# Performance work log

Hardware: AMD Instinct MI355X
Metric: run time of the kernel (lower is better)

## Reference

```python
import jax, jax.numpy as jnp
import numpy as np

B, L, HID, NH = 8, 512, 768, 12
D = HID // NH
T_HOP, T_EDGE = 32, 64


def setup_inputs() -> dict:
    key = jax.random.key(0)
    ks = jax.random.split(key, 18)
    f = lambda k, s, sc=1.0: jax.random.normal(k, s, dtype=jnp.float32) * sc
    return {
        "x": f(ks[0], (B, L, HID)),
        "query_hop_emb": f(ks[1], (T_HOP, HID), 0.05),
        "query_edge_emb": f(ks[2], (T_EDGE, HID), 0.05),
        "key_hop_emb": f(ks[3], (T_HOP, HID), 0.05),
        "key_edge_emb": f(ks[4], (T_EDGE, HID), 0.05),
        "value_hop_emb": f(ks[5], (T_HOP, HID), 0.05),
        "value_edge_emb": f(ks[6], (T_EDGE, HID), 0.05),
        "hop": jax.random.randint(ks[7], (B, L, L), 0, T_HOP, dtype=jnp.int32),
        "edge_matrix": jax.random.randint(ks[8], (B, L, L), 0, T_EDGE, dtype=jnp.int32),
        "Wq": f(ks[9], (HID, HID), 0.02), "bq": f(ks[10], (HID,), 0.02),
        "Wk": f(ks[11], (HID, HID), 0.02), "bk": f(ks[12], (HID,), 0.02),
        "Wv": f(ks[13], (HID, HID), 0.02), "bv": f(ks[14], (HID,), 0.02),
        "Wo": f(ks[15], (HID, HID), 0.02), "bo": f(ks[16], (HID,), 0.02),
    }


def reference(x, query_hop_emb, query_edge_emb, key_hop_emb, key_edge_emb,
              value_hop_emb, value_edge_emb, hop, edge_matrix,
              Wq, bq, Wk, bk, Wv, bv, Wo, bo):
    b, l, _ = x.shape
    scale = 1.0 / np.sqrt(D).astype(np.float32)
    heads = lambda t: t.reshape(b, l, NH, D).transpose(0, 2, 1, 3)  # [B,H,L,D]
    emb = lambda t: t.reshape(-1, NH, D)                             # [T,H,D]

    q = heads(x @ Wq + bq)
    k = heads(x @ Wk + bk)
    v = heads(x @ Wv + bv)

    hop_idx = jnp.broadcast_to(hop[:, None], (b, NH, l, l))
    edge_idx = jnp.broadcast_to(edge_matrix[:, None], (b, NH, l, l))

    def bias(t, e, idx):
        # project onto type embeddings then gather per (i,j) type: [B,H,L,L]
        proj = jnp.einsum('bhld,thd->bhlt', t, emb(e))
        return jnp.take_along_axis(proj, idx, axis=3)

    scores = jnp.einsum('bhld,bhmd->bhlm', q, k)
    scores = scores + bias(q, query_hop_emb, hop_idx) + bias(q, query_edge_emb, edge_idx)
    scores = scores + bias(k, key_hop_emb, hop_idx) + bias(k, key_edge_emb, edge_idx)
    att = jax.nn.softmax(scores * scale, axis=3)

    def scatter_by_type(a, idx, T):
        # re-aggregate attention weights per hop/edge type: [B,H,L,T]
        bi = jnp.arange(b)[:, None, None, None]
        hi = jnp.arange(NH)[None, :, None, None]
        li = jnp.arange(l)[None, None, :, None]
        return jnp.zeros((b, NH, l, T), a.dtype).at[bi, hi, li, idx].add(a)

    out = jnp.einsum('bhlm,bhmd->bhld', att, v)
    out = out + jnp.einsum('bhlt,thd->bhld', scatter_by_type(att, hop_idx, T_HOP), emb(value_hop_emb))
    out = out + jnp.einsum('bhlt,thd->bhld', scatter_by_type(att, edge_idx, T_EDGE), emb(value_edge_emb))

    out = out.transpose(0, 2, 1, 3).reshape(b, l, NH * D)
    return out @ Wo + bo
```

## Files before the change

kernel.cpp:

```cpp
#include <hip/hip_runtime.h>
#include <stdint.h>

#define B_   8
#define L_   512
#define HID_ 768
#define NH_  12
#define D_   64
#define BH_  96
#define TT_  96

typedef __attribute__((ext_vector_type(8))) short short8;
typedef __attribute__((ext_vector_type(4))) float fv4;

#define MFMA16(a, b, c) __builtin_amdgcn_mfma_f32_16x16x32_bf16((a), (b), (c), 0, 0, 0)

__device__ __forceinline__ float bf2f(uint16_t h) {
  union { uint32_t u; float f; } c; c.u = ((uint32_t)h) << 16; return c.f;
}
__device__ __forceinline__ uint16_t f2bf(float x) {
  union { float f; uint32_t u; } c; c.f = x;
  uint32_t r = (c.u + 0x7FFFu + ((c.u >> 16) & 1u)) >> 16;
  return (uint16_t)r;
}
__device__ __forceinline__ float clampf(float v, float lim) {
  return fminf(fmaxf(v, -lim), lim);
}

__device__ __forceinline__ void gld_lds16(const uint16_t* g, uint16_t* lds) {
  __builtin_amdgcn_global_load_lds(
      (const __attribute__((address_space(1))) uint32_t*)(uintptr_t)g,
      (__attribute__((address_space(3))) uint32_t*)(uintptr_t)lds, 16, 0, 0);
}

__device__ __forceinline__ int detect_fp32(const void* xraw) {
  const uint16_t* r = (const uint16_t*)xraw;
  int cnt = 0;
#pragma unroll
  for (int j = 0; j < 16; j++) {
    uint16_t u = r[2 * j];
    int e = (u >> 7) & 0xFF;
    if (u != 0 && e >= 100 && e <= 140) cnt++;
  }
  return cnt < 10;
}

#define SEG_X    0
#define SEG_QH   3145728
#define SEG_QE   3170304
#define SEG_KH   3219456
#define SEG_KE   3244032
#define SEG_VH   3293184
#define SEG_VE   3317760
#define SEG_BQ   3366912
#define SEG_BK   3367680
#define SEG_BV   3368448
#define SEG_BO   3369216
#define SEG_END  3369984
#define SEG_VET  3369984
#define SEG_PK   3443712
#define SEG_ALL  5540864

__global__ __launch_bounds__(256) void convert_all(
    const void* __restrict__ x, const void* __restrict__ qh,
    const void* __restrict__ qe, const void* __restrict__ kh,
    const void* __restrict__ ke, const void* __restrict__ vh,
    const void* __restrict__ ve, const void* __restrict__ b0,
    const void* __restrict__ b1, const void* __restrict__ b2,
    const void* __restrict__ b3, const int* __restrict__ hop,
    const int* __restrict__ edge, uint16_t* __restrict__ dst,
    uint16_t* __restrict__ VET, uint16_t* __restrict__ PK) {
  const int gid = blockIdx.x * 256 + threadIdx.x;
  if (gid >= SEG_ALL) return;
  const int f = detect_fp32(x);
  if (gid >= SEG_PK) {
    const int g = gid - SEG_PK;
    PK[g] = (uint16_t)((hop[g] & 31) | ((edge[g] & 63) << 8));
    return;
  }
  if (gid >= SEG_VET) {
    const int g = gid - SEG_VET;
    const int t = g % TT_;
    const int d = (g / TT_) % D_;
    const int hh = g / (TT_ * D_);
    const void* src = (t < 32) ? vh : ve;
    const size_t idx = (size_t)(t < 32 ? t : t - 32) * HID_ + hh * D_ + d;
    VET[g] = f ? f2bf(((const float*)src)[idx]) : ((const uint16_t*)src)[idx];
    return;
  }
  const void* src;
  int local;
  if (gid < SEG_QH)      { src = x;  local = gid - SEG_X; }
  else if (gid < SEG_QE) { src = qh; local = gid - SEG_QH; }
  else if (gid < SEG_KH) { src = qe; local = gid - SEG_QE; }
  else if (gid < SEG_KE) { src = kh; local = gid - SEG_KH; }
  else if (gid < SEG_VH) { src = ke; local = gid - SEG_KE; }
  else if (gid < SEG_VE) { src = vh; local = gid - SEG_VH; }
  else if (gid < SEG_BQ) { src = ve; local = gid - SEG_VE; }
  else if (gid < SEG_BK) { src = b0; local = gid - SEG_BQ; }
  else if (gid < SEG_BV) { src = b1; local = gid - SEG_BK; }
  else if (gid < SEG_BO) { src = b2; local = gid - SEG_BV; }
  else                   { src = b3; local = gid - SEG_BO; }
  if (f)
    dst[gid] = f2bf(((const float*)src)[local]);
  else
    dst[gid] = ((const uint16_t*)src)[local];
}

__global__ __launch_bounds__(256) void tr_any4(
    const void* __restrict__ s0, const void* __restrict__ s1,
    const void* __restrict__ s2, const void* __restrict__ s3,
    uint16_t* __restrict__ dstbase) {
  __shared__ uint16_t t[32][33];
  const int z = blockIdx.z;
  const void* src = (z == 0) ? s0 : (z == 1) ? s1 : (z == 2) ? s2 : s3;
  uint16_t* dst = dstbase + (size_t)z * (768 * 768);
  const int fp32 = detect_fp32(s0);
  const int tx = threadIdx.x, ty = threadIdx.y;
  const int r0 = blockIdx.y * 32, c0 = blockIdx.x * 32;
#pragma unroll
  for (int k = 0; k < 4; k++) {
    size_t idx = (size_t)(r0 + ty + k * 8) * 768 + c0 + tx;
    t[ty + k * 8][tx] =
        fp32 ? f2bf(((const float*)src)[idx]) : ((const uint16_t*)src)[idx];
  }
  __syncthreads();
#pragma unroll
  for (int k = 0; k < 4; k++)
    dst[(size_t)(c0 + ty + k * 8) * 768 + r0 + tx] = t[tx][ty + k * 8];
}

__global__ __launch_bounds__(256) void gemm128(
    const uint16_t* __restrict__ A,
    const uint16_t* __restrict__ BT0, const uint16_t* __restrict__ BT1,
    const uint16_t* __restrict__ BT2,
    const uint16_t* __restrict__ bias0, const uint16_t* __restrict__ bias1,
    const uint16_t* __restrict__ bias2,
    uint16_t* __restrict__ out, uint16_t* __restrict__ vt) {
  const int z = blockIdx.z;
  const uint16_t* BT = (z == 0) ? BT0 : (z == 1) ? BT1 : BT2;
  const uint16_t* bias = (z == 0) ? bias0 : (z == 1) ? bias1 : bias2;

  __shared__ __align__(16) uint16_t As[128 * 32];
  __shared__ __align__(16) uint16_t Bs[128 * 32];

  const int tid = threadIdx.x;
  const int lane = tid & 63, quad = lane >> 4, l16 = lane & 15;
  const int w = tid >> 6, wm = w & 1, wn = w >> 1;
  const int m0 = blockIdx.x * 128, n0 = blockIdx.y * 128;

  fv4 acc[4][4];
#pragma unroll
  for (int i = 0; i < 4; i++)
#pragma unroll
    for (int j = 0; j < 4; j++) acc[i][j] = (fv4){0.f, 0.f, 0.f, 0.f};

  const int c0 = tid, c1 = tid + 256;
  const int r0 = c0 >> 2, g0 = (c0 & 3) ^ ((r0 >> 1) & 3);
  const int r1 = c1 >> 2, g1 = (c1 & 3) ^ ((r1 >> 1) & 3);
  const uint16_t* A0 = A + (size_t)(m0 + r0) * HID_ + g0 * 8;
  const uint16_t* A1 = A + (size_t)(m0 + r1) * HID_ + g1 * 8;
  const uint16_t* B0 = BT + (size_t)(n0 + r0) * HID_ + g0 * 8;
  const uint16_t* B1 = BT + (size_t)(n0 + r1) * HID_ + g1 * 8;
  uint16_t* lA0 = &As[c0 * 8];
  uint16_t* lA1 = &As[c1 * 8];
  uint16_t* lB0 = &Bs[c0 * 8];
  uint16_t* lB1 = &Bs[c1 * 8];

  int aoff[4], boff[4];
#pragma unroll
  for (int mi = 0; mi < 4; mi++) {
    int row = wm * 64 + mi * 16 + l16;
    aoff[mi] = row * 32 + (quad ^ ((row >> 1) & 3)) * 8;
  }
#pragma unroll
  for (int ni = 0; ni < 4; ni++) {
    int row = wn * 64 + ni * 16 + l16;
    boff[ni] = row * 32 + (quad ^ ((row >> 1) & 3)) * 8;
  }

  for (int k0 = 0; k0 < HID_; k0 += 32) {
    __syncthreads();
    gld_lds16(A0 + k0, lA0);
    gld_lds16(A1 + k0, lA1);
    gld_lds16(B0 + k0, lB0);
    gld_lds16(B1 + k0, lB1);
    __syncthreads();
    short8 af[4], bf[4];
#pragma unroll
    for (int mi = 0; mi < 4; mi++) af[mi] = *(const short8*)&As[aoff[mi]];
#pragma unroll
    for (int ni = 0; ni < 4; ni++) bf[ni] = *(const short8*)&Bs[boff[ni]];
#pragma unroll
    for (int mi = 0; mi < 4; mi++)
#pragma unroll
      for (int ni = 0; ni < 4; ni++)
        acc[mi][ni] = MFMA16(af[mi], bf[ni], acc[mi][ni]);
  }

#pragma unroll
  for (int mi = 0; mi < 4; mi++) {
#pragma unroll
    for (int ni = 0; ni < 4; ni++) {
      const int gn = n0 + wn * 64 + ni * 16 + l16;
      const float bv = bf2f(bias[gn]);
      const int gm0 = m0 + wm * 64 + mi * 16 + quad * 4;
      if (z == 2) {
        const int bb = gm0 >> 9, ll0 = gm0 & 511;
        const int hh = gn >> 6, dd = gn & 63;
        ushort4 pk;
        pk.x = f2bf(clampf(acc[mi][ni][0] + bv, 1e4f));
        pk.y = f2bf(clampf(acc[mi][ni][1] + bv, 1e4f));
        pk.z = f2bf(clampf(acc[mi][ni][2] + bv, 1e4f));
        pk.w = f2bf(clampf(acc[mi][ni][3] + bv, 1e4f));
        *(ushort4*)&vt[(((size_t)(bb * NH_ + hh)) * D_ + dd) * L_ + ll0] = pk;
      } else {
#pragma unroll
        for (int r = 0; r < 4; r++) {
          const int gm = gm0 + r;
          const float fval = clampf(acc[mi][ni][r] + bv, 1e4f);
          uint16_t* O = out + (size_t)z * ((size_t)BH_ * L_ * D_);
          const int bb = gm >> 9, ll = gm & 511, hh = gn >> 6, dd = gn & 63;
          O[(((size_t)(bb * NH_ + hh)) * L_ + ll) * D_ + dd] = f2bf(fval);
        }
      }
    }
  }
}

__global__ __launch_bounds__(256) void gemm64o(
    const uint16_t* __restrict__ A, const uint16_t* __restrict__ BT,
    const uint16_t* __restrict__ bias, float* __restrict__ out) {
  __shared__ __align__(16) uint16_t As[64 * 32];
  __shared__ __align__(16) uint16_t Bs[64 * 32];

  const int tid = threadIdx.x;
  const int lane = tid & 63, quad = lane >> 4, l16 = lane & 15;
  const int w = tid >> 6, wm = w & 1, wn = w >> 1;
  const int m0 = blockIdx.x * 64, n0 = blockIdx.y * 64;

  fv4 acc[2][2];
#pragma unroll
  for (int i = 0; i < 2; i++)
#pragma unroll
    for (int j = 0; j < 2; j++) acc[i][j] = (fv4){0.f, 0.f, 0.f, 0.f};

  const int c0 = tid;
  const int r0 = c0 >> 2, g0 = (c0 & 3) ^ ((r0 >> 1) & 3);
  const uint16_t* A0 = A + (size_t)(m0 + r0) * HID_ + g0 * 8;
  const uint16_t* B0 = BT + (size_t)(n0 + r0) * HID_ + g0 * 8;
  uint16_t* lA0 = &As[c0 * 8];
  uint16_t* lB0 = &Bs[c0 * 8];

  int aoff[2], boff[2];
#pragma unroll
  for (int mi = 0; mi < 2; mi++) {
    int row = wm * 32 + mi * 16 + l16;
    aoff[mi] = row * 32 + (quad ^ ((row >> 1) & 3)) * 8;
  }
#pragma unroll
  for (int ni = 0; ni < 2; ni++) {
    int row = wn * 32 + ni * 16 + l16;
    boff[ni] = row * 32 + (quad ^ ((row >> 1) & 3)) * 8;
  }

  for (int k0 = 0; k0 < HID_; k0 += 32) {
    __syncthreads();
    gld_lds16(A0 + k0, lA0);
    gld_lds16(B0 + k0, lB0);
    __syncthreads();
    short8 af[2], bf[2];
#pragma unroll
    for (int mi = 0; mi < 2; mi++) af[mi] = *(const short8*)&As[aoff[mi]];
#pragma unroll
    for (int ni = 0; ni < 2; ni++) bf[ni] = *(const short8*)&Bs[boff[ni]];
#pragma unroll
    for (int mi = 0; mi < 2; mi++)
#pragma unroll
      for (int ni = 0; ni < 2; ni++)
        acc[mi][ni] = MFMA16(af[mi], bf[ni], acc[mi][ni]);
  }

#pragma unroll
  for (int mi = 0; mi < 2; mi++) {
#pragma unroll
    for (int ni = 0; ni < 2; ni++) {
      const int gn = n0 + wn * 32 + ni * 16 + l16;
      const float bv = bf2f(bias[gn]);
#pragma unroll
      for (int r = 0; r < 4; r++) {
        const int gm = m0 + wm * 32 + mi * 16 + quad * 4 + r;
        out[(size_t)gm * HID_ + gn] = clampf(acc[mi][ni][r] + bv, 1e4f);
      }
    }
  }
}

#define SCALE_FX 4194304.f
#define INV_SCALE_FX 2.38418579e-7f
#define UBC 40.f

__global__ __launch_bounds__(256) void attn_kernel(
    const uint16_t* __restrict__ Q, const uint16_t* __restrict__ Km,
    const uint16_t* __restrict__ Vt,
    const uint16_t* __restrict__ qh, const uint16_t* __restrict__ qe,
    const uint16_t* __restrict__ kh, const uint16_t* __restrict__ ke,
    const uint16_t* __restrict__ VET, const uint16_t* __restrict__ PK,
    uint16_t* __restrict__ AO) {
  const int n = blockIdx.x;
  const int h = n % NH_;
  const int t2 = n / NH_;
  const int it = t2 & 7, b = t2 >> 3;
  const int bh = b * NH_ + h;
  const int i0 = it * 64;
  const int tid = threadIdx.x;
  const int w = tid >> 6, lane = tid & 63, quad = lane >> 4, l16 = lane & 15;
  const int gi = i0 + w * 16;

  __shared__ uint16_t cbs[4][16][98];
  __shared__ unsigned bkt[4][16][97];
  __shared__ __align__(16) uint16_t Pw[4][16][72];

  for (int k = lane; k < 16 * 97; k += 64) (&bkt[0][0][0])[w * 16 * 97 + k] = 0u;

  const size_t qkb = (size_t)bh * (L_ * D_);
  short8 a0 = *(const short8*)&Q[qkb + (size_t)(gi + l16) * D_ + quad * 8];
  short8 a1 = *(const short8*)&Q[qkb + (size_t)(gi + l16) * D_ + 32 + quad * 8];
  short8 kq0 = *(const short8*)&Km[qkb + (size_t)(gi + l16) * D_ + quad * 8];
  short8 kq1 =
      *(const short8*)&Km[qkb + (size_t)(gi + l16) * D_ + 32 + quad * 8];

  float hx[4] = {-1e30f, -1e30f, -1e30f, -1e30f};
  float ex[4] = {-1e30f, -1e30f, -1e30f, -1e30f};
#pragma unroll
  for (int nt = 0; nt < 6; nt++) {
    const uint16_t* eq;
    const uint16_t* ek;
    int t;
    if (nt < 2) { eq = qh; ek = kh; t = nt * 16 + l16; }
    else        { eq = qe; ek = ke; t = (nt - 2) * 16 + l16; }
    const size_t eb0 = (size_t)t * HID_ + h * D_;
    short8 bq0 = *(const short8*)&eq[eb0 + quad * 8];
    short8 bq1 = *(const short8*)&eq[eb0 + 32 + quad * 8];
    short8 bk0 = *(const short8*)&ek[eb0 + quad * 8];
    short8 bk1 = *(const short8*)&ek[eb0 + 32 + quad * 8];
    fv4 cc = (fv4){0.f, 0.f, 0.f, 0.f};
    cc = MFMA16(a0, bq0, cc);
    cc = MFMA16(a1, bq1, cc);
    cc = MFMA16(kq0, bk0, cc);
    cc = MFMA16(kq1, bk1, cc);
#pragma unroll
    for (int r = 0; r < 4; r++) {
      const float cv = clampf(cc[r], 1e4f);
      cbs[w][quad * 4 + r][nt * 16 + l16] = f2bf(cv);
      if (nt < 2) hx[r] = fmaxf(hx[r], cv);
      else        ex[r] = fmaxf(ex[r], cv);
    }
  }

  float mx[4];
#pragma unroll
  for (int r = 0; r < 4; r++) {
    float mh = hx[r], me = ex[r];
    mh = fmaxf(mh, __shfl_xor(mh, 1, 16));
    mh = fmaxf(mh, __shfl_xor(mh, 2, 16));
    mh = fmaxf(mh, __shfl_xor(mh, 4, 16));
    mh = fmaxf(mh, __shfl_xor(mh, 8, 16));
    me = fmaxf(me, __shfl_xor(me, 1, 16));
    me = fmaxf(me, __shfl_xor(me, 2, 16));
    me = fmaxf(me, __shfl_xor(me, 4, 16));
    me = fmaxf(me, __shfl_xor(me, 8, 16));
    mx[r] = mh + me + UBC;
  }

  const uint16_t* pkb = PK + ((size_t)(b * L_) + gi) * L_;
  const size_t vtb = (size_t)bh * (D_ * L_);

  fv4 oacc[4];
#pragma unroll
  for (int ni = 0; ni < 4; ni++) oacc[ni] = (fv4){0.f, 0.f, 0.f, 0.f};
  float lsr[4] = {0.f, 0.f, 0.f, 0.f};

  for (int jc = 0; jc < 8; jc++) {
    fv4 sacc[4];
#pragma unroll
    for (int ni = 0; ni < 4; ni++) {
      const int key = jc * 64 + ni * 16 + l16;
      short8 kb0 = *(const short8*)&Km[qkb + (size_t)key * D_ + quad * 8];
      short8 kb1 = *(const short8*)&Km[qkb + (size_t)key * D_ + 32 + quad * 8];
      fv4 a = (fv4){0.f, 0.f, 0.f, 0.f};
      a = MFMA16(a0, kb0, a);
      sacc[ni] = MFMA16(a1, kb1, a);
    }
#pragma unroll
    for (int ni = 0; ni < 4; ni++) {
#pragma unroll
      for (int r = 0; r < 4; r++) {
        const int row = quad * 4 + r;
        const uint32_t pk = pkb[(size_t)row * L_ + jc * 64 + ni * 16 + l16];
        const int th = pk & 31, te = pk >> 8;
        float s = sacc[ni][r] + bf2f(cbs[w][row][th]) +
                  bf2f(cbs[w][row][32 + te]);
        const float p = __expf((s - mx[r]) * 0.125f);
        lsr[r] += p;
        const unsigned pfx = (unsigned)(p * SCALE_FX + 0.5f);
        atomicAdd(&bkt[w][row][th], pfx);
        atomicAdd(&bkt[w][row][32 + te], pfx);
        Pw[w][row][ni * 16 + l16] = f2bf(p);
      }
    }
#pragma unroll
    for (int kc = 0; kc < 2; kc++) {
      short8 pa = *(const short8*)&Pw[w][l16][kc * 32 + quad * 8];
#pragma unroll
      for (int ni = 0; ni < 4; ni++) {
        short8 vb = *(const short8*)&Vt[vtb + (size_t)(ni * 16 + l16) * L_ +
                                        jc * 64 + kc * 32 + quad * 8];
        oacc[ni] = MFMA16(pa, vb, oacc[ni]);
      }
    }
  }

  const uint16_t* vet = VET + (size_t)h * D_ * TT_;
#pragma unroll
  for (int kc = 0; kc < 3; kc++) {
    short8 pa;
#pragma unroll
    for (int j = 0; j < 8; j++)
      pa[j] = (short)f2bf((float)bkt[w][l16][kc * 32 + quad * 8 + j] *
                          INV_SCALE_FX);
#pragma unroll
    for (int ni = 0; ni < 4; ni++) {
      short8 vb =
          *(const short8*)&vet[(size_t)(ni * 16 + l16) * TT_ + kc * 32 +
                               quad * 8];
      oacc[ni] = MFMA16(pa, vb, oacc[ni]);
    }
  }

  float linv[4];
#pragma unroll
  for (int r = 0; r < 4; r++) {
    float s = lsr[r];
    s += __shfl_xor(s, 1, 16);
    s += __shfl_xor(s, 2, 16);
    s += __shfl_xor(s, 4, 16);
    s += __shfl_xor(s, 8, 16);
    linv[r] = 1.f / s;
  }

#pragma unroll
  for (int ni = 0; ni < 4; ni++)
#pragma unroll
    for (int r = 0; r < 4; r++) {
      const int i = gi + quad * 4 + r;
      AO[(((size_t)b * L_ + i) * NH_ + h) * D_ + ni * 16 + l16] =
          f2bf(oacc[ni][r] * linv[r]);
    }
}

extern "C" void kernel_launch(void* const* d_in, const int* in_sizes, int n_in,
                              void* d_out, int out_size, void* d_ws,
                              size_t ws_size, hipStream_t stream) {
  const void* x_raw = d_in[0];
  const int* hop    = (const int*)d_in[7];
  const int* edge   = (const int*)d_in[8];

  char* ws = (char*)d_ws;
  uint16_t* QKV = (uint16_t*)(ws);
  uint16_t* Qp  = QKV;
  uint16_t* Kp  = QKV + (size_t)BH_ * L_ * D_;
  uint16_t* Vtp = (uint16_t*)(ws + 18874368);
  uint16_t* PKp = (uint16_t*)(ws + 25165824);
  uint16_t* AO  = (uint16_t*)(ws + 44040192);
  uint16_t* WTq = (uint16_t*)(ws + 50331648);
  uint16_t* WTk = WTq + 768 * 768;
  uint16_t* WTv = WTk + 768 * 768;
  uint16_t* WTo = WTv + 768 * 768;
  uint16_t* CAN = (uint16_t*)(ws + 55050240);
  uint16_t* VET = (uint16_t*)(ws + 61790208);

  uint16_t* xc  = CAN + SEG_X;
  uint16_t* qhc = CAN + SEG_QH;
  uint16_t* qec = CAN + SEG_QE;
  uint16_t* khc = CAN + SEG_KH;
  uint16_t* kec = CAN + SEG_KE;
  uint16_t* bqc = CAN + SEG_BQ;
  uint16_t* bkc = CAN + SEG_BK;
  uint16_t* bvc = CAN + SEG_BV;
  uint16_t* boc = CAN + SEG_BO;

  convert_all<<<(SEG_ALL + 255) / 256, 256, 0, stream>>>(
      x_raw, d_in[1], d_in[2], d_in[3], d_in[4], d_in[5], d_in[6],
      d_in[10], d_in[12], d_in[14], d_in[16], hop, edge, CAN, VET, PKp);

  dim3 tb(32, 8, 1);
  tr_any4<<<dim3(24, 24, 4), tb, 0, stream>>>(d_in[9], d_in[11], d_in[13],
                                              d_in[15], WTq);

  gemm128<<<dim3(32, 6, 3), 256, 0, stream>>>(xc, WTq, WTk, WTv, bqc, bkc,
                                              bvc, QKV, Vtp);

  attn_kernel<<<768, 256, 0, stream>>>(Qp, Kp, Vtp, qhc, qec, khc, kec, VET,
                                       PKp, AO);

  gemm64o<<<dim3(64, 12), 256, 0, stream>>>(AO, WTo, boc, (float*)d_out);
}
```

Measured before the change: 236.3 us.

## Pre-swizzle packed hop/edge indices to lane order for vectorized loads in attention

The conversion kernel now writes the packed hop/edge type indices in a layout that matches the attention kernel's MFMA lane/register ownership, so each lane gets its 16 indices per key chunk with two 16-byte loads instead of 16 scattered 2-byte loads. The softmax/bucket loop is split into phases (decode indices, gather biases, exponentiate, then atomics and P writes) to expose more independent work. A launch-bounds occupancy hint of 3 blocks is also added. The costs are a scattered write pattern in the conversion kernel and possible register pressure from the 16-element arrays under the occupancy constraint.

```diff
diff --git a/kernel.cpp b/kernel.cpp
--- a/kernel.cpp
+++ b/kernel.cpp
@@ -68,13 +68,22 @@
     const void* __restrict__ b1, const void* __restrict__ b2,
     const void* __restrict__ b3, const int* __restrict__ hop,
     const int* __restrict__ edge, uint16_t* __restrict__ dst,
-    uint16_t* __restrict__ VET, uint16_t* __restrict__ PK) {
+    uint16_t* __restrict__ VET, uint16_t* __restrict__ PKs) {
   const int gid = blockIdx.x * 256 + threadIdx.x;
   if (gid >= SEG_ALL) return;
   const int f = detect_fp32(x);
   if (gid >= SEG_PK) {
     const int g = gid - SEG_PK;
-    PK[g] = (uint16_t)((hop[g] & 31) | ((edge[g] & 63) << 8));
+    const int j = g & 511;
+    const int i = (g >> 9) & 511;
+    const int b = g >> 18;
+    const int it = i >> 6, w = (i >> 4) & 3, quad = (i >> 2) & 3, r = i & 3;
+    const int jc = j >> 6, ni = (j >> 4) & 3, l16 = j & 15;
+    const int lane = quad * 16 + l16;
+    const size_t didx =
+        ((((size_t)(b * 8 + it) * 4 + w) * 8 + jc) * 64 + lane) * 16 + r * 4 +
+        ni;
+    PKs[didx] = (uint16_t)((hop[g] & 31) | ((edge[g] & 63) << 8));
     return;
   }
   if (gid >= SEG_VET) {
@@ -299,28 +308,28 @@
 #define INV_SCALE_FX 2.38418579e-7f
 #define UBC 40.f
 
-__global__ __launch_bounds__(256) void attn_kernel(
+__global__ __launch_bounds__(256, 3) void attn_kernel(
     const uint16_t* __restrict__ Q, const uint16_t* __restrict__ Km,
     const uint16_t* __restrict__ Vt,
     const uint16_t* __restrict__ qh, const uint16_t* __restrict__ qe,
     const uint16_t* __restrict__ kh, const uint16_t* __restrict__ ke,
-    const uint16_t* __restrict__ VET, const uint16_t* __restrict__ PK,
+    const uint16_t* __restrict__ VET, const uint16_t* __restrict__ PKs,
     uint16_t* __restrict__ AO) {
   const int n = blockIdx.x;
   const int h = n % NH_;
   const int t2 = n / NH_;
   const int it = t2 & 7, b = t2 >> 3;
   const int bh = b * NH_ + h;
-  const int i0 = it * 64;
   const int tid = threadIdx.x;
   const int w = tid >> 6, lane = tid & 63, quad = lane >> 4, l16 = lane & 15;
-  const int gi = i0 + w * 16;
+  const int gi = it * 64 + w * 16;
 
   __shared__ uint16_t cbs[4][16][98];
   __shared__ unsigned bkt[4][16][97];
   __shared__ __align__(16) uint16_t Pw[4][16][72];
 
-  for (int k = lane; k < 16 * 97; k += 64) (&bkt[0][0][0])[w * 16 * 97 + k] = 0u;
+  for (int k = lane; k < 16 * 97; k += 64)
+    (&bkt[0][0][0])[w * 16 * 97 + k] = 0u;
 
   const size_t qkb = (size_t)bh * (L_ * D_);
   short8 a0 = *(const short8*)&Q[qkb + (size_t)(gi + l16) * D_ + quad * 8];
@@ -372,7 +381,8 @@
     mx[r] = mh + me + UBC;
   }
 
-  const uint16_t* pkb = PK + ((size_t)(b * L_) + gi) * L_;
+  const uint16_t* pkw =
+      PKs + (((size_t)(b * 8 + it) * 4 + w) * 8) * (64 * 16);
   const size_t vtb = (size_t)bh * (D_ * L_);
 
   fv4 oacc[4];
@@ -381,6 +391,9 @@
   float lsr[4] = {0.f, 0.f, 0.f, 0.f};
 
   for (int jc = 0; jc < 8; jc++) {
+    short8 pk0 = *(const short8*)&pkw[jc * 1024 + lane * 16];
+    short8 pk1 = *(const short8*)&pkw[jc * 1024 + lane * 16 + 8];
+
     fv4 sacc[4];
 #pragma unroll
     for (int ni = 0; ni < 4; ni++) {
@@ -391,23 +404,38 @@
       a = MFMA16(a0, kb0, a);
       sacc[ni] = MFMA16(a1, kb1, a);
     }
-#pragma unroll
-    for (int ni = 0; ni < 4; ni++) {
-#pragma unroll
-      for (int r = 0; r < 4; r++) {
-        const int row = quad * 4 + r;
-        const uint32_t pk = pkb[(size_t)row * L_ + jc * 64 + ni * 16 + l16];
-        const int th = pk & 31, te = pk >> 8;
-        float s = sacc[ni][r] + bf2f(cbs[w][row][th]) +
-                  bf2f(cbs[w][row][32 + te]);
-        const float p = __expf((s - mx[r]) * 0.125f);
-        lsr[r] += p;
-        const unsigned pfx = (unsigned)(p * SCALE_FX + 0.5f);
-        atomicAdd(&bkt[w][row][th], pfx);
-        atomicAdd(&bkt[w][row][32 + te], pfx);
-        Pw[w][row][ni * 16 + l16] = f2bf(p);
-      }
-    }
+
+    int thv[16], tev[16];
+#pragma unroll
+    for (int k = 0; k < 16; k++) {
+      const uint32_t pk = (uint16_t)((k < 8) ? pk0[k] : pk1[k - 8]);
+      thv[k] = pk & 31;
+      tev[k] = (pk >> 8) & 63;
+    }
+    float bsum[16];
+#pragma unroll
+    for (int k = 0; k < 16; k++) {
+      const int row = quad * 4 + (k >> 2);
+      bsum[k] = bf2f(cbs[w][row][thv[k]]) + bf2f(cbs[w][row][32 + tev[k]]);
+    }
+    float pv[16];
+#pragma unroll
+    for (int k = 0; k < 16; k++) {
+      const int r = k >> 2;
+      const float s = sacc[k & 3][r] + bsum[k];
+      const float p = __expf((s - mx[r]) * 0.125f);
+      pv[k] = p;
+      lsr[r] += p;
+    }
+#pragma unroll
+    for (int k = 0; k < 16; k++) {
+      const int row = quad * 4 + (k >> 2);
+      const unsigned pfx = (unsigned)(pv[k] * SCALE_FX + 0.5f);
+      atomicAdd(&bkt[w][row][thv[k]], pfx);
+      atomicAdd(&bkt[w][row][32 + tev[k]], pfx);
+      Pw[w][row][(k & 3) * 16 + l16] = f2bf(pv[k]);
+    }
+
 #pragma unroll
     for (int kc = 0; kc < 2; kc++) {
       short8 pa = *(const short8*)&Pw[w][l16][kc * 32 + quad * 8];
@@ -470,7 +498,7 @@
   uint16_t* Qp  = QKV;
   uint16_t* Kp  = QKV + (size_t)BH_ * L_ * D_;
   uint16_t* Vtp = (uint16_t*)(ws + 18874368);
-  uint16_t* PKp = (uint16_t*)(ws + 25165824);
+  uint16_t* PKs = (uint16_t*)(ws + 25165824);
   uint16_t* AO  = (uint16_t*)(ws + 44040192);
   uint16_t* WTq = (uint16_t*)(ws + 50331648);
   uint16_t* WTk = WTq + 768 * 768;
@@ -491,7 +519,7 @@
 
   convert_all<<<(SEG_ALL + 255) / 256, 256, 0, stream>>>(
       x_raw, d_in[1], d_in[2], d_in[3], d_in[4], d_in[5], d_in[6],
-      d_in[10], d_in[12], d_in[14], d_in[16], hop, edge, CAN, VET, PKp);
+      d_in[10], d_in[12], d_in[14], d_in[16], hop, edge, CAN, VET, PKs);
 
   dim3 tb(32, 8, 1);
   tr_any4<<<dim3(24, 24, 4), tb, 0, stream>>>(d_in[9], d_in[11], d_in[13],
@@ -501,7 +529,7 @@
                                               bvc, QKV, Vtp);
 
   attn_kernel<<<768, 256, 0, stream>>>(Qp, Kp, Vtp, qhc, qec, khc, kec, VET,
-                                       PKp, AO);
+                                       PKs, AO);
 
   gemm64o<<<dim3(64, 12), 256, 0, stream>>>(AO, WTo, boc, (float*)d_out);
 }
```

Result: faster. 225.6 us (-4.5%).
